# Kernel tuning notes

Hardware: AMD Instinct MI355X
Metric: run time of the kernel (lower is better)

Reference implementation:

```python
import jax, jax.numpy as jnp
import numpy as np

# Model dims (match init_kwargs)
D_MODEL = 768
EXPAND = 2
HEADDIM = 64
D_STATE = 64
D_CONV = 4
D_INNER = EXPAND * D_MODEL            # 1536 (== d_ssm, d_mlp = 0)
NHEADS = D_INNER // HEADDIM           # 24
CONV_DIM_PH = HEADDIM + 2 * D_STATE   # 192
CONV_DIM = NHEADS * CONV_DIM_PH       # 4608
D_IN_PROJ = D_INNER + CONV_DIM + NHEADS  # z + xBC + dt (d_mlp=0)

DT_MIN, DT_MAX = 1e-3, 1e-1


def setup_inputs() -> dict:
    key = jax.random.key(0)
    ks = jax.random.split(key, 12)
    B, L = 2, 2048
    s = 0.02
    # dt_bias init as in the torch module: inv_softplus of dt ~ loguniform(dt_min, dt_max)
    dt = jnp.exp(jax.random.uniform(ks[8], (NHEADS,)) * (np.log(DT_MAX) - np.log(DT_MIN)) + np.log(DT_MIN))
    dt = jnp.clip(dt, 1e-4, None)
    dt_bias = dt + jnp.log(-jnp.expm1(-dt))
    A_log = jnp.log(jax.random.uniform(ks[9], (NHEADS,), minval=1.0, maxval=16.0))
    return {
        "u": jax.random.normal(ks[0], (B, L, D_MODEL), jnp.float32),
        "W_in": jax.random.normal(ks[1], (D_IN_PROJ, D_MODEL), jnp.float32) * s,
        "conv_w": jax.random.normal(ks[2], (CONV_DIM, 1, D_CONV), jnp.float32) * 0.1,
        "conv_b": jnp.zeros((CONV_DIM,), jnp.float32),
        "R_x": jax.random.normal(ks[3], (NHEADS, HEADDIM, HEADDIM), jnp.float32) * 0.01,
        "R_B": jax.random.normal(ks[4], (NHEADS, D_STATE, HEADDIM), jnp.float32) * 0.01,
        "R_C": jax.random.normal(ks[5], (NHEADS, D_STATE, HEADDIM), jnp.float32) * 0.01,
        "R_dt": jax.random.normal(ks[6], (NHEADS, HEADDIM), jnp.float32) * 0.01,
        "dt_bias": dt_bias,
        "A_log": A_log,
        "D": jnp.ones((NHEADS, HEADDIM), jnp.float32),
        "W_out": jax.random.normal(ks[7], (D_MODEL, D_INNER), jnp.float32) * s,
    }


def reference(u, W_in, conv_w, conv_b, R_x, R_B, R_C, R_dt, dt_bias, A_log, D, W_out):
    B, L, _ = u.shape
    silu = jax.nn.silu

    # in_proj: split into SSM gate z, conv input xBC, dt pre-activation (d_mlp = 0)
    zxbcdt = u @ W_in.T                              # (B, L, D_IN_PROJ)
    z = zxbcdt[..., :D_INNER]                        # (B, L, d_ssm)
    xBC_in = zxbcdt[..., D_INNER:D_INNER + CONV_DIM] # (B, L, conv_dim)
    dt_raw = zxbcdt[..., D_INNER + CONV_DIM:]        # (B, L, NH)

    # causal depthwise conv1d (left-pad d_conv-1, truncate to L)
    xc = jax.lax.conv_general_dilated(
        xBC_in.transpose(0, 2, 1), conv_w,
        window_strides=(1,), padding=[(D_CONV - 1, 0)],
        dimension_numbers=("NCH", "OIH", "NCH"),
        feature_group_count=CONV_DIM) + conv_b[None, :, None]
    xBC_u = xc.transpose(0, 2, 1).reshape(B, L, NHEADS, CONV_DIM_PH)

    A = -jnp.exp(A_log)  # (NH,)

    def step(carry, inp):
        state, y_prev = carry            # (B,NH,DH,N), (B,NH,DH)
        xBC_t, dtr_t = inp               # (B,NH,DH+2N), (B,NH)
        x_u = xBC_t[..., :HEADDIM]
        B_u = xBC_t[..., HEADDIM:HEADDIM + D_STATE]
        C_u = xBC_t[..., HEADDIM + D_STATE:]
        # recurrent feedback of y_prev into x/B/C (pre-activation), then silu
        x = silu(x_u + jnp.einsum('hpq,bhq->bhp', R_x, y_prev))
        Bm = silu(B_u + jnp.einsum('hnq,bhq->bhn', R_B, y_prev))
        Cm = silu(C_u + jnp.einsum('hnq,bhq->bhn', R_C, y_prev))
        dt = jax.nn.softplus(dtr_t + jnp.einsum('hp,bhp->bh', R_dt, y_prev) + dt_bias)  # (B,NH)
        dA = jnp.exp(dt * A)             # (B,NH)
        state = state * dA[..., None, None] + (dt[..., None] * x)[..., None] * Bm[:, :, None, :]
        y = jnp.einsum('bhpn,bhn->bhp', state, Cm) + D * x   # (B,NH,DH)
        return (state, y), y

    state0 = jnp.zeros((B, NHEADS, HEADDIM, D_STATE), u.dtype)
    y0 = jnp.zeros((B, NHEADS, HEADDIM), u.dtype)
    xs = (xBC_u.transpose(1, 0, 2, 3), dt_raw.transpose(1, 0, 2))
    _, ys = jax.lax.scan(step, (state0, y0), xs)

    y = ys.transpose(1, 0, 2, 3)                              # (B,L,NH,DH)
    y = y * silu(z.reshape(B, L, NHEADS, HEADDIM))            # SSM gating
    out = y.reshape(B, L, D_INNER) @ W_out.T                  # (B,L,d_model)
    return out
```

## Files before the change

### kernel.cpp

```cpp
#include <hip/hip_runtime.h>

#define B_SZ    2
#define LSEQ    2048
#define DMODEL  768
#define DINNER  1536
#define NHEADS  24
#define HD      64
#define CDPH    192
#define CONVDIM 4608
#define DIP     6168
#define MROWS   (B_SZ*LSEQ)

typedef float f2 __attribute__((ext_vector_type(2)));
typedef float f32x4 __attribute__((ext_vector_type(4)));
typedef short bf16x8 __attribute__((ext_vector_type(8)));

__device__ __forceinline__ float siluf(float x) {
    return x / (1.0f + __expf(-x));
}

#define WBAR() do { asm volatile("s_waitcnt lgkmcnt(0)" ::: "memory"); \
                    __builtin_amdgcn_s_barrier();                      \
                    asm volatile("" ::: "memory"); } while (0)

__device__ __forceinline__ float redux4(float v) {
    float a = v, b = v;
    asm("v_permlane16_swap_b32 %0, %1" : "+v"(a), "+v"(b));
    const float s = a + b;
    float c = s, d = s;
    asm("v_permlane32_swap_b32 %0, %1" : "+v"(c), "+v"(d));
    return c + d;
}

__device__ __forceinline__ ushort f2bf(float v) {
    uint u = __float_as_uint(v);
    return (ushort)((u + 0x7FFFu + ((u >> 16) & 1u)) >> 16);
}
__device__ __forceinline__ float bf2f(ushort h) {
    return __uint_as_float(((uint)h) << 16);
}

__global__ __launch_bounds__(256) void gemm_nt_split(
    const float* __restrict__ A, const float* __restrict__ B,
    float* __restrict__ C, int M, int N, int K)
{
    __shared__ ushort As_hi[128][56];
    __shared__ ushort As_lo[128][56];
    __shared__ ushort Bs_hi[128][56];
    __shared__ ushort Bs_lo[128][56];

    const int ntn = (N + 127) >> 7;
    const int bm = blockIdx.x / ntn;
    const int bn = blockIdx.x - bm * ntn;
    const int m0 = bm << 7, n0 = bn << 7;
    const int tid = threadIdx.x;
    const int wid = tid >> 6;
    const int l = tid & 63;
    const int wm = wid >> 1, wn = wid & 1;
    const int lr = l & 15;
    const int kq = l >> 4;

    const int srow = tid >> 1;
    const int scol = (tid & 1) << 4;
    const float* Ap = A + (size_t)(m0 + srow) * K + scol;
    const bool bok = (n0 + srow) < N;
    const float* Bp = B + (size_t)(n0 + srow) * K + scol;

    f32x4 acc[4][4];
#pragma unroll
    for (int i = 0; i < 4; ++i)
#pragma unroll
        for (int j = 0; j < 4; ++j) acc[i][j] = f32x4{0.f, 0.f, 0.f, 0.f};

    for (int k0 = 0; k0 < K; k0 += 32) {
        float av[16], bv[16];
#pragma unroll
        for (int q = 0; q < 4; ++q) {
            const float4 t = *(const float4*)(Ap + k0 + q * 4);
            av[q*4+0] = t.x; av[q*4+1] = t.y; av[q*4+2] = t.z; av[q*4+3] = t.w;
        }
#pragma unroll
        for (int q = 0; q < 4; ++q) {
            float4 t = make_float4(0.f, 0.f, 0.f, 0.f);
            if (bok) t = *(const float4*)(Bp + k0 + q * 4);
            bv[q*4+0] = t.x; bv[q*4+1] = t.y; bv[q*4+2] = t.z; bv[q*4+3] = t.w;
        }
        __syncthreads();
#pragma unroll
        for (int q = 0; q < 16; ++q) {
            const ushort ah = f2bf(av[q]);
            As_hi[srow][scol + q] = ah;
            As_lo[srow][scol + q] = f2bf(av[q] - bf2f(ah));
            const ushort bh = f2bf(bv[q]);
            Bs_hi[srow][scol + q] = bh;
            Bs_lo[srow][scol + q] = f2bf(bv[q] - bf2f(bh));
        }
        __syncthreads();

        bf16x8 ah[4], al[4], bh[4], bl[4];
#pragma unroll
        for (int f = 0; f < 4; ++f) {
            const int ra = wm * 64 + f * 16 + lr;
            ah[f] = *(const bf16x8*)&As_hi[ra][kq * 8];
            al[f] = *(const bf16x8*)&As_lo[ra][kq * 8];
            const int rb = wn * 64 + f * 16 + lr;
            bh[f] = *(const bf16x8*)&Bs_hi[rb][kq * 8];
            bl[f] = *(const bf16x8*)&Bs_lo[rb][kq * 8];
        }
#pragma unroll
        for (int i = 0; i < 4; ++i)
#pragma unroll
            for (int j = 0; j < 4; ++j) {
                acc[i][j] = __builtin_amdgcn_mfma_f32_16x16x32_bf16(
                    ah[i], bh[j], acc[i][j], 0, 0, 0);
                acc[i][j] = __builtin_amdgcn_mfma_f32_16x16x32_bf16(
                    ah[i], bl[j], acc[i][j], 0, 0, 0);
                acc[i][j] = __builtin_amdgcn_mfma_f32_16x16x32_bf16(
                    al[i], bh[j], acc[i][j], 0, 0, 0);
            }
    }

#pragma unroll
    for (int i = 0; i < 4; ++i) {
#pragma unroll
        for (int j = 0; j < 4; ++j) {
            const int n = n0 + wn * 64 + j * 16 + lr;
            if (n < N) {
#pragma unroll
                for (int rg = 0; rg < 4; ++rg) {
                    const int m = m0 + wm * 64 + i * 16 + kq * 4 + rg;
                    C[(size_t)m * N + n] = acc[i][j][rg];
                }
            }
        }
    }
}

__global__ __launch_bounds__(256, 1) void mamba_scan7(
    const float* __restrict__ zx,
    const float* __restrict__ conv_w,
    const float* __restrict__ conv_b,
    const float* __restrict__ R_x,
    const float* __restrict__ R_B,
    const float* __restrict__ R_C,
    const float* __restrict__ R_dt,
    const float* __restrict__ dt_bias,
    const float* __restrict__ A_log,
    const float* __restrict__ Dvec,
    float* __restrict__ yz)
{
    const int b = blockIdx.x / NHEADS;
    const int h = blockIdx.x % NHEADS;
    const int tid = threadIdx.x;
    const int w = tid >> 6;
    const int l = tid & 63;
    const int g = l >> 4;
    const int r = l & 15;
    const int p = (w << 4) + r;

    __shared__ __attribute__((aligned(16))) float ybuf[64];
    __shared__ __attribute__((aligned(16))) float Bml[64];
    __shared__ __attribute__((aligned(16))) float Cml[64];

    f2 Rx2[8], Rb2[8], Rc2[8], Rd2[8];
    {
        const size_t ro = ((size_t)h * 64 + p) * 64 + (g << 4);
#pragma unroll
        for (int q = 0; q < 4; ++q) {
            const float4 v = *(const float4*)(R_x + ro + q * 4);
            Rx2[q*2] = f2{v.x, v.y}; Rx2[q*2+1] = f2{v.z, v.w};
        }
#pragma unroll
        for (int q = 0; q < 4; ++q) {
            const float4 v = *(const float4*)(R_B + ro + q * 4);
            Rb2[q*2] = f2{v.x, v.y}; Rb2[q*2+1] = f2{v.z, v.w};
        }
#pragma unroll
        for (int q = 0; q < 4; ++q) {
            const float4 v = *(const float4*)(R_C + ro + q * 4);
            Rc2[q*2] = f2{v.x, v.y}; Rc2[q*2+1] = f2{v.z, v.w};
        }
#pragma unroll
        for (int q = 0; q < 4; ++q) {
            const float4 v = *(const float4*)(R_dt + h * 64 + (g << 4) + q * 4);
            Rd2[q*2] = f2{v.x, v.y}; Rd2[q*2+1] = f2{v.z, v.w};
        }
    }
    const float Aval = -__expf(A_log[h]);
    const float bias = dt_bias[h];
    const float Dp   = Dvec[h * 64 + p];

    float wx0, wx1, wx2, wx3, wb0, wb1, wb2, wb3, wc0, wc1, wc2, wc3;
    float cbx, cbB, cbC;
    {
        const float* cw = conv_w + (size_t)h * CDPH * 4;
        const float4 vx = *(const float4*)(cw + (size_t)p * 4);
        const float4 vb = *(const float4*)(cw + (size_t)(64 + p) * 4);
        const float4 vc = *(const float4*)(cw + (size_t)(128 + p) * 4);
        wx0 = vx.x; wx1 = vx.y; wx2 = vx.z; wx3 = vx.w;
        wb0 = vb.x; wb1 = vb.y; wb2 = vb.z; wb3 = vb.w;
        wc0 = vc.x; wc1 = vc.y; wc2 = vc.z; wc3 = vc.w;
        cbx = conv_b[h * CDPH + p];
        cbB = conv_b[h * CDPH + 64 + p];
        cbC = conv_b[h * CDPH + 128 + p];
    }
    float hx0 = 0.f, hx1 = 0.f, hx2 = 0.f;
    float hB0 = 0.f, hB1 = 0.f, hB2 = 0.f;
    float hC0 = 0.f, hC1 = 0.f, hC2 = 0.f;

    const float* xbc = zx + (size_t)b * LSEQ * DIP + DINNER + h * CDPH;
    const float* zb  = zx + (size_t)b * LSEQ * DIP + h * HD;
    const float* dtp = zx + (size_t)b * LSEQ * DIP + DINNER + CONVDIM + h;
    float* yzb = yz + (size_t)b * LSEQ * DINNER + h * HD;

    f2 st2[8];
#pragma unroll
    for (int q = 0; q < 8; ++q) st2[q] = f2{0.f, 0.f};

    if (g == 0) ybuf[p] = 0.f;
    __syncthreads();

    float vx_c = xbc[p], vB_c = xbc[64 + p], vC_c = xbc[128 + p];
    float z_c = zb[p];
    float dtr_c = dtp[0];
    int off = DIP;

    for (int t = 0; t < LSEQ; ++t) {
        const float xcx = fmaf(wx3, vx_c, fmaf(wx2, hx2, fmaf(wx1, hx1, fmaf(wx0, hx0, cbx))));
        const float xcB = fmaf(wb3, vB_c, fmaf(wb2, hB2, fmaf(wb1, hB1, fmaf(wb0, hB0, cbB))));
        const float xcC = fmaf(wc3, vC_c, fmaf(wc2, hC2, fmaf(wc1, hC1, fmaf(wc0, hC0, cbC))));
        hx0 = hx1; hx1 = hx2; hx2 = vx_c;
        hB0 = hB1; hB1 = hB2; hB2 = vB_c;
        hC0 = hC1; hC1 = hC2; hC2 = vC_c;

        const float vx_n = xbc[off + p];
        const float vB_n = xbc[off + 64 + p];
        const float vC_n = xbc[off + 128 + p];
        const float z_n  = zb[off + p];
        const float dtr_n = dtp[off];
        const float zg = siluf(z_c);

        const float4* yb4 = (const float4*)(ybuf + (g << 4));
        f2 ax2 = {0.f, 0.f}, ab2 = {0.f, 0.f}, ac2 = {0.f, 0.f}, ad2 = {0.f, 0.f};
#pragma unroll
        for (int qq = 0; qq < 4; ++qq) {
            const float4 y4 = yb4[qq];
            const f2 ylo = {y4.x, y4.y}, yhi = {y4.z, y4.w};
            ax2 += Rx2[qq*2] * ylo; ax2 += Rx2[qq*2+1] * yhi;
            ab2 += Rb2[qq*2] * ylo; ab2 += Rb2[qq*2+1] * yhi;
            ac2 += Rc2[qq*2] * ylo; ac2 += Rc2[qq*2+1] * yhi;
            ad2 += Rd2[qq*2] * ylo; ad2 += Rd2[qq*2+1] * yhi;
        }
        const float ax = ax2.x + ax2.y, ab = ab2.x + ab2.y;
        const float ac = ac2.x + ac2.y, ad = ad2.x + ad2.y;

        const float Bm = siluf(xcB + redux4(ab));
        const float Cm = siluf(xcC + redux4(ac));
        if (g == 0) { Bml[p] = Bm; Cml[p] = Cm; }
        WBAR();

        const float4* bm4 = (const float4*)(Bml + (g << 4));
        const float4* cm4 = (const float4*)(Cml + (g << 4));
        const float4 bA = bm4[0], bB = bm4[1], bC = bm4[2], bD = bm4[3];
        const float4 cA = cm4[0], cB = cm4[1], cC = cm4[2], cD = cm4[3];

        const float xv = siluf(xcx + redux4(ax));
        const float dv = dtr_c + redux4(ad) + bias;
        const float dtv = (dv > 15.f) ? dv : __logf(1.f + __expf(dv));
        const float dAv = __expf(dtv * Aval);
        const float kx = dtv * xv;

        const f2 dA2 = {dAv, dAv};
        const f2 kx2 = {kx, kx};
        f2 bmv[8], cmv[8];
        bmv[0] = f2{bA.x, bA.y}; bmv[1] = f2{bA.z, bA.w};
        bmv[2] = f2{bB.x, bB.y}; bmv[3] = f2{bB.z, bB.w};
        bmv[4] = f2{bC.x, bC.y}; bmv[5] = f2{bC.z, bC.w};
        bmv[6] = f2{bD.x, bD.y}; bmv[7] = f2{bD.z, bD.w};
        cmv[0] = f2{cA.x, cA.y}; cmv[1] = f2{cA.z, cA.w};
        cmv[2] = f2{cB.x, cB.y}; cmv[3] = f2{cB.z, cB.w};
        cmv[4] = f2{cC.x, cC.y}; cmv[5] = f2{cC.z, cC.w};
        cmv[6] = f2{cD.x, cD.y}; cmv[7] = f2{cD.z, cD.w};
        f2 yp2 = {0.f, 0.f};
#pragma unroll
        for (int q = 0; q < 8; ++q) {
            st2[q] = st2[q] * dA2 + kx2 * bmv[q];
            yp2 += st2[q] * cmv[q];
        }
        const float ynew = redux4(yp2.x + yp2.y) + Dp * xv;

        if (g == 0) {
            ybuf[p] = ynew;
            yzb[p] = ynew * zg;
        }
        WBAR();

        vx_c = vx_n; vB_c = vB_n; vC_c = vC_n; z_c = z_n; dtr_c = dtr_n;
        off += DIP;
        yzb += DINNER;
    }
}

extern "C" void kernel_launch(void* const* d_in, const int* in_sizes, int n_in,
                              void* d_out, int out_size, void* d_ws, size_t ws_size,
                              hipStream_t stream) {
    const float* u       = (const float*)d_in[0];
    const float* W_in    = (const float*)d_in[1];
    const float* conv_w  = (const float*)d_in[2];
    const float* conv_b  = (const float*)d_in[3];
    const float* R_x     = (const float*)d_in[4];
    const float* R_B     = (const float*)d_in[5];
    const float* R_C     = (const float*)d_in[6];
    const float* R_dt    = (const float*)d_in[7];
    const float* dt_bias = (const float*)d_in[8];
    const float* A_log   = (const float*)d_in[9];
    const float* Dv      = (const float*)d_in[10];
    const float* W_out   = (const float*)d_in[11];
    float* out = (float*)d_out;

    float* zx = (float*)d_ws;
    float* yz = zx + (size_t)MROWS * DIP;

    {
        const int M = MROWS, N = DIP, K = DMODEL;
        const int grid = (M / 128) * ((N + 127) / 128);
        gemm_nt_split<<<grid, 256, 0, stream>>>(u, W_in, zx, M, N, K);
    }
    mamba_scan7<<<B_SZ * NHEADS, 256, 0, stream>>>(
        zx, conv_w, conv_b, R_x, R_B, R_C, R_dt, dt_bias, A_log, Dv, yz);
    {
        const int M = MROWS, N = DMODEL, K = DINNER;
        const int grid = (M / 128) * ((N + 127) / 128);
        gemm_nt_split<<<grid, 256, 0, stream>>>(yz, W_out, out, M, N, K);
    }
}
```

Baseline: 2.002 ms.

## Pre-split GEMM operands into bf16 hi/lo planes and use packed FMA in scan

Adds a conversion kernel that splits u, W_in and W_out into bf16 high/low planes once per call in workspace. The GEMMs then load those planes directly, so the per-tile float-to-bf16 split is no longer repeated by every tile that reads the same data. The scan kernel's paired float math is rewritten with inline v_pk_fma/v_pk_mul assembly. The cost is three extra launches and extra global traffic for the planes. The new path needs a larger workspace and falls back to the old GEMM if it is too small.

After: 2.203 ms. 10.0% more time.

```diff
diff --git a/kernel.cpp b/kernel.cpp
--- a/kernel.cpp
+++ b/kernel.cpp
@@ -14,6 +14,7 @@
 typedef float f2 __attribute__((ext_vector_type(2)));
 typedef float f32x4 __attribute__((ext_vector_type(4)));
 typedef short bf16x8 __attribute__((ext_vector_type(8)));
+typedef unsigned short us8 __attribute__((ext_vector_type(8)));
 
 __device__ __forceinline__ float siluf(float x) {
     return x / (1.0f + __expf(-x));
@@ -22,6 +23,17 @@
 #define WBAR() do { asm volatile("s_waitcnt lgkmcnt(0)" ::: "memory"); \
                     __builtin_amdgcn_s_barrier();                      \
                     asm volatile("" ::: "memory"); } while (0)
+
+__device__ __forceinline__ void pk_fma(f2& d, const f2 a, const f2 b) {
+    asm("v_pk_fma_f32 %0, %1, %2, %0 op_sel:[0,0,0] op_sel_hi:[1,1,1]"
+        : "+v"(d) : "v"(a), "v"(b));
+}
+__device__ __forceinline__ f2 pk_mul(const f2 a, const f2 b) {
+    f2 d;
+    asm("v_pk_mul_f32 %0, %1, %2 op_sel:[0,0] op_sel_hi:[1,1]"
+        : "=v"(d) : "v"(a), "v"(b));
+    return d;
+}
 
 __device__ __forceinline__ float redux4(float v) {
     float a = v, b = v;
@@ -40,8 +52,30 @@
     return __uint_as_float(((uint)h) << 16);
 }
 
+__global__ __launch_bounds__(256) void cvt_split(
+    const float* __restrict__ in, ushort* __restrict__ hi,
+    ushort* __restrict__ lo, int n4)
+{
+    int i = blockIdx.x * blockDim.x + threadIdx.x;
+    const int stride = gridDim.x * blockDim.x;
+    for (; i < n4; i += stride) {
+        const float4 v = ((const float4*)in)[i];
+        ushort4 h, l;
+        h.x = f2bf(v.x); l.x = f2bf(v.x - bf2f(h.x));
+        h.y = f2bf(v.y); l.y = f2bf(v.y - bf2f(h.y));
+        h.z = f2bf(v.z); l.z = f2bf(v.z - bf2f(h.z));
+        h.w = f2bf(v.w); l.w = f2bf(v.w - bf2f(h.w));
+        ((ushort4*)hi)[i] = h;
+        ((ushort4*)lo)[i] = l;
+    }
+}
+
+template<int MODE>
 __global__ __launch_bounds__(256) void gemm_nt_split(
-    const float* __restrict__ A, const float* __restrict__ B,
+    const float* __restrict__ A,
+    const ushort* __restrict__ Ahi, const ushort* __restrict__ Alo,
+    const float* __restrict__ B_,
+    const ushort* __restrict__ Bhi, const ushort* __restrict__ Blo,
     float* __restrict__ C, int M, int N, int K)
 {
     __shared__ ushort As_hi[128][56];
@@ -62,9 +96,7 @@
 
     const int srow = tid >> 1;
     const int scol = (tid & 1) << 4;
-    const float* Ap = A + (size_t)(m0 + srow) * K + scol;
     const bool bok = (n0 + srow) < N;
-    const float* Bp = B + (size_t)(n0 + srow) * K + scol;
 
     f32x4 acc[4][4];
 #pragma unroll
@@ -72,51 +104,89 @@
 #pragma unroll
         for (int j = 0; j < 4; ++j) acc[i][j] = f32x4{0.f, 0.f, 0.f, 0.f};
 
+    const size_t arow = (size_t)(m0 + srow) * K + scol;
+    const size_t brow = (size_t)(n0 + srow) * K + scol;
+
     for (int k0 = 0; k0 < K; k0 += 32) {
-        float av[16], bv[16];
-#pragma unroll
-        for (int q = 0; q < 4; ++q) {
-            const float4 t = *(const float4*)(Ap + k0 + q * 4);
-            av[q*4+0] = t.x; av[q*4+1] = t.y; av[q*4+2] = t.z; av[q*4+3] = t.w;
-        }
-#pragma unroll
-        for (int q = 0; q < 4; ++q) {
-            float4 t = make_float4(0.f, 0.f, 0.f, 0.f);
-            if (bok) t = *(const float4*)(Bp + k0 + q * 4);
-            bv[q*4+0] = t.x; bv[q*4+1] = t.y; bv[q*4+2] = t.z; bv[q*4+3] = t.w;
+        us8 ah0, ah1, al0, al1;
+        float av[16];
+        if constexpr (MODE >= 2) {
+            ah0 = *(const us8*)(Ahi + arow + k0);
+            ah1 = *(const us8*)(Ahi + arow + k0 + 8);
+            al0 = *(const us8*)(Alo + arow + k0);
+            al1 = *(const us8*)(Alo + arow + k0 + 8);
+        } else {
+#pragma unroll
+            for (int q = 0; q < 4; ++q) {
+                const float4 t = *(const float4*)(A + arow + k0 + q * 4);
+                av[q*4+0] = t.x; av[q*4+1] = t.y;
+                av[q*4+2] = t.z; av[q*4+3] = t.w;
+            }
+        }
+        us8 bh0, bh1, bl0, bl1;
+        float bv[16];
+        if constexpr (MODE >= 1) {
+            bh0 = us8{}; bh1 = us8{}; bl0 = us8{}; bl1 = us8{};
+            if (bok) {
+                bh0 = *(const us8*)(Bhi + brow + k0);
+                bh1 = *(const us8*)(Bhi + brow + k0 + 8);
+                bl0 = *(const us8*)(Blo + brow + k0);
+                bl1 = *(const us8*)(Blo + brow + k0 + 8);
+            }
+        } else {
+#pragma unroll
+            for (int q = 0; q < 4; ++q) {
+                float4 t = make_float4(0.f, 0.f, 0.f, 0.f);
+                if (bok) t = *(const float4*)(B_ + brow + k0 + q * 4);
+                bv[q*4+0] = t.x; bv[q*4+1] = t.y;
+                bv[q*4+2] = t.z; bv[q*4+3] = t.w;
+            }
         }
         __syncthreads();
-#pragma unroll
-        for (int q = 0; q < 16; ++q) {
-            const ushort ah = f2bf(av[q]);
-            As_hi[srow][scol + q] = ah;
-            As_lo[srow][scol + q] = f2bf(av[q] - bf2f(ah));
-            const ushort bh = f2bf(bv[q]);
-            Bs_hi[srow][scol + q] = bh;
-            Bs_lo[srow][scol + q] = f2bf(bv[q] - bf2f(bh));
+        if constexpr (MODE >= 2) {
+            *(us8*)&As_hi[srow][scol] = ah0; *(us8*)&As_hi[srow][scol + 8] = ah1;
+            *(us8*)&As_lo[srow][scol] = al0; *(us8*)&As_lo[srow][scol + 8] = al1;
+        } else {
+#pragma unroll
+            for (int q = 0; q < 16; ++q) {
+                const ushort ah = f2bf(av[q]);
+                As_hi[srow][scol + q] = ah;
+                As_lo[srow][scol + q] = f2bf(av[q] - bf2f(ah));
+            }
+        }
+        if constexpr (MODE >= 1) {
+            *(us8*)&Bs_hi[srow][scol] = bh0; *(us8*)&Bs_hi[srow][scol + 8] = bh1;
+            *(us8*)&Bs_lo[srow][scol] = bl0; *(us8*)&Bs_lo[srow][scol + 8] = bl1;
+        } else {
+#pragma unroll
+            for (int q = 0; q < 16; ++q) {
+                const ushort bh = f2bf(bv[q]);
+                Bs_hi[srow][scol + q] = bh;
+                Bs_lo[srow][scol + q] = f2bf(bv[q] - bf2f(bh));
+            }
         }
         __syncthreads();
 
-        bf16x8 ah[4], al[4], bh[4], bl[4];
+        bf16x8 ahf[4], alf[4], bhf[4], blf[4];
 #pragma unroll
         for (int f = 0; f < 4; ++f) {
             const int ra = wm * 64 + f * 16 + lr;
-            ah[f] = *(const bf16x8*)&As_hi[ra][kq * 8];
-            al[f] = *(const bf16x8*)&As_lo[ra][kq * 8];
+            ahf[f] = *(const bf16x8*)&As_hi[ra][kq * 8];
+            alf[f] = *(const bf16x8*)&As_lo[ra][kq * 8];
             const int rb = wn * 64 + f * 16 + lr;
-            bh[f] = *(const bf16x8*)&Bs_hi[rb][kq * 8];
-            bl[f] = *(const bf16x8*)&Bs_lo[rb][kq * 8];
+            bhf[f] = *(const bf16x8*)&Bs_hi[rb][kq * 8];
+            blf[f] = *(const bf16x8*)&Bs_lo[rb][kq * 8];
         }
 #pragma unroll
         for (int i = 0; i < 4; ++i)
 #pragma unroll
             for (int j = 0; j < 4; ++j) {
                 acc[i][j] = __builtin_amdgcn_mfma_f32_16x16x32_bf16(
-                    ah[i], bh[j], acc[i][j], 0, 0, 0);
+                    ahf[i], bhf[j], acc[i][j], 0, 0, 0);
                 acc[i][j] = __builtin_amdgcn_mfma_f32_16x16x32_bf16(
-                    ah[i], bl[j], acc[i][j], 0, 0, 0);
+                    ahf[i], blf[j], acc[i][j], 0, 0, 0);
                 acc[i][j] = __builtin_amdgcn_mfma_f32_16x16x32_bf16(
-                    al[i], bh[j], acc[i][j], 0, 0, 0);
+                    alf[i], bhf[j], acc[i][j], 0, 0, 0);
             }
     }
 
@@ -136,7 +206,7 @@
     }
 }
 
-__global__ __launch_bounds__(256, 1) void mamba_scan7(
+__global__ __launch_bounds__(256, 1) void mamba_scan8(
     const float* __restrict__ zx,
     const float* __restrict__ conv_w,
     const float* __restrict__ conv_b,
@@ -246,10 +316,10 @@
         for (int qq = 0; qq < 4; ++qq) {
             const float4 y4 = yb4[qq];
             const f2 ylo = {y4.x, y4.y}, yhi = {y4.z, y4.w};
-            ax2 += Rx2[qq*2] * ylo; ax2 += Rx2[qq*2+1] * yhi;
-            ab2 += Rb2[qq*2] * ylo; ab2 += Rb2[qq*2+1] * yhi;
-            ac2 += Rc2[qq*2] * ylo; ac2 += Rc2[qq*2+1] * yhi;
-            ad2 += Rd2[qq*2] * ylo; ad2 += Rd2[qq*2+1] * yhi;
+            pk_fma(ax2, Rx2[qq*2], ylo); pk_fma(ax2, Rx2[qq*2+1], yhi);
+            pk_fma(ab2, Rb2[qq*2], ylo); pk_fma(ab2, Rb2[qq*2+1], yhi);
+            pk_fma(ac2, Rc2[qq*2], ylo); pk_fma(ac2, Rc2[qq*2+1], yhi);
+            pk_fma(ad2, Rd2[qq*2], ylo); pk_fma(ad2, Rd2[qq*2+1], yhi);
         }
         const float ax = ax2.x + ax2.y, ab = ab2.x + ab2.y;
         const float ac = ac2.x + ac2.y, ad = ad2.x + ad2.y;
@@ -284,8 +354,10 @@
         f2 yp2 = {0.f, 0.f};
 #pragma unroll
         for (int q = 0; q < 8; ++q) {
-            st2[q] = st2[q] * dA2 + kx2 * bmv[q];
-            yp2 += st2[q] * cmv[q];
+            f2 rr = pk_mul(kx2, bmv[q]);
+            pk_fma(rr, st2[q], dA2);
+            st2[q] = rr;
+            pk_fma(yp2, st2[q], cmv[q]);
         }
         const float ynew = redux4(yp2.x + yp2.y) + Dp * xv;
 
@@ -318,19 +390,50 @@
     const float* W_out   = (const float*)d_in[11];
     float* out = (float*)d_out;
 
+    const size_t ZXF = (size_t)MROWS * DIP;
+    const size_t YZF = (size_t)MROWS * DINNER;
+    const size_t UE  = (size_t)MROWS * DMODEL;
+    const size_t WIE = (size_t)DIP * DMODEL;
+    const size_t WOE = (size_t)DMODEL * DINNER;
+    const size_t PLANESF = (UE + WIE + WOE);
+    const size_t NEEDF = ZXF + YZF + PLANESF;
+
     float* zx = (float*)d_ws;
-    float* yz = zx + (size_t)MROWS * DIP;
+    float* yz = zx + ZXF;
+    const bool pre = ws_size >= NEEDF * sizeof(float);
+
+    ushort *uhi = nullptr, *ulo = nullptr, *wihi = nullptr, *wilo = nullptr,
+           *wohi = nullptr, *wolo = nullptr;
+    if (pre) {
+        float* pb = yz + YZF;
+        uhi  = (ushort*)pb;            ulo  = uhi + UE;
+        wihi = (ushort*)(pb + UE);     wilo = wihi + WIE;
+        wohi = (ushort*)(pb + UE + WIE); wolo = wohi + WOE;
+        cvt_split<<<512, 256, 0, stream>>>(u, uhi, ulo, (int)(UE / 4));
+        cvt_split<<<512, 256, 0, stream>>>(W_in, wihi, wilo, (int)(WIE / 4));
+        cvt_split<<<512, 256, 0, stream>>>(W_out, wohi, wolo, (int)(WOE / 4));
+    }
 
     {
         const int M = MROWS, N = DIP, K = DMODEL;
         const int grid = (M / 128) * ((N + 127) / 128);
-        gemm_nt_split<<<grid, 256, 0, stream>>>(u, W_in, zx, M, N, K);
-    }
-    mamba_scan7<<<B_SZ * NHEADS, 256, 0, stream>>>(
+        if (pre)
+            gemm_nt_split<2><<<grid, 256, 0, stream>>>(
+                nullptr, uhi, ulo, nullptr, wihi, wilo, zx, M, N, K);
+        else
+            gemm_nt_split<0><<<grid, 256, 0, stream>>>(
+                u, nullptr, nullptr, W_in, nullptr, nullptr, zx, M, N, K);
+    }
+    mamba_scan8<<<B_SZ * NHEADS, 256, 0, stream>>>(
         zx, conv_w, conv_b, R_x, R_B, R_C, R_dt, dt_bias, A_log, Dv, yz);
     {
         const int M = MROWS, N = DMODEL, K = DINNER;
         const int grid = (M / 128) * ((N + 127) / 128);
-        gemm_nt_split<<<grid, 256, 0, stream>>>(yz, W_out, out, M, N, K);
-    }
-}
+        if (pre)
+            gemm_nt_split<1><<<grid, 256, 0, stream>>>(
+                yz, nullptr, nullptr, nullptr, wohi, wolo, out, M, N, K);
+        else
+            gemm_nt_split<0><<<grid, 256, 0, stream>>>(
+                yz, nullptr, nullptr, W_out, nullptr, nullptr, out, M, N, K);
+    }
+}
```
